# Kernel tuning notes

Measured on AMD Instinct MI355X. Metric: run time of the kernel, lower is better.

Reference implementation:

```python
import jax, jax.numpy as jnp
import numpy as np

INPUT_DIM = 1024
HIDDEN_DIM = 2048
LATENT_DIM = 256
NUM_EMBEDDINGS = 8192
COMMITMENT_COST = 0.25
BATCH = 16384


def setup_inputs() -> dict:
    key = jax.random.key(0)
    ks = jax.random.split(key, 10)
    def lin(k, fan_in, fan_out):
        # torch nn.Linear default init: U(-1/sqrt(fan_in), 1/sqrt(fan_in))
        bound = 1.0 / np.sqrt(fan_in)
        kw, kb = jax.random.split(k)
        W = jax.random.uniform(kw, (fan_in, fan_out), jnp.float32, -bound, bound)
        b = jax.random.uniform(kb, (fan_out,), jnp.float32, -bound, bound)
        return W, b
    enc_w1, enc_b1 = lin(ks[0], INPUT_DIM, HIDDEN_DIM)
    enc_w2, enc_b2 = lin(ks[1], HIDDEN_DIM, LATENT_DIM)
    dec_w1, dec_b1 = lin(ks[2], LATENT_DIM, HIDDEN_DIM)
    dec_w2, dec_b2 = lin(ks[3], HIDDEN_DIM, INPUT_DIM)
    # codebook init: U(-1/K, 1/K)
    codebook = jax.random.uniform(ks[4], (NUM_EMBEDDINGS, LATENT_DIM), jnp.float32,
                                  -1.0 / NUM_EMBEDDINGS, 1.0 / NUM_EMBEDDINGS)
    x = jax.random.uniform(ks[5], (BATCH, INPUT_DIM), jnp.float32)
    return {"x": x,
            "enc_w1": enc_w1, "enc_b1": enc_b1, "enc_w2": enc_w2, "enc_b2": enc_b2,
            "codebook": codebook,
            "dec_w1": dec_w1, "dec_b1": dec_b1, "dec_w2": dec_w2, "dec_b2": dec_b2}


def reference(x, enc_w1, enc_b1, enc_w2, enc_b2, codebook,
              dec_w1, dec_b1, dec_w2, dec_b2):
    # Encoder: relu(x W1 + b1) W2 + b2 -> z [N, latent]
    h = jax.nn.relu(x @ enc_w1 + enc_b1)
    z = h @ enc_w2 + enc_b2

    # Vector quantizer: squared-L2 distances to codebook [N, K]
    d = (jnp.sum(z * z, axis=1, keepdims=True)
         + jnp.sum(codebook * codebook, axis=1)
         - 2.0 * (z @ codebook.T))
    idx = jnp.argmin(d, axis=1)          # [N] int
    z_q = codebook[idx]                   # gather [N, latent]

    vq_loss = jnp.mean((jax.lax.stop_gradient(z_q) - z) ** 2)
    commit_loss = COMMITMENT_COST * jnp.mean((z_q - jax.lax.stop_gradient(z)) ** 2)
    loss = vq_loss + commit_loss

    # straight-through estimator
    z_q = z + jax.lax.stop_gradient(z_q - z)

    # Decoder: sigmoid(relu(z_q Wd1 + bd1) Wd2 + bd2)
    hd = jax.nn.relu(z_q @ dec_w1 + dec_b1)
    x_recon = jax.nn.sigmoid(hd @ dec_w2 + dec_b2)
    return (x_recon, loss)
```

## Files before the change

kernel.cpp:

```cpp
#include <hip/hip_runtime.h>
#include <math.h>

typedef unsigned short u16;
typedef __bf16 bf16x8 __attribute__((ext_vector_type(8)));
typedef float  f32x4  __attribute__((ext_vector_type(4)));

constexpr int B_  = 16384;
constexpr int DIN = 1024;
constexpr int DH  = 2048;
constexpr int DL  = 256;
constexpr int NE  = 8192;

__device__ __forceinline__ u16 f2bf(float f) {
    union { float f; unsigned u; } v; v.f = f;
    unsigned r = v.u + 0x7fffu + ((v.u >> 16) & 1u);
    return (u16)(r >> 16);
}
__device__ __forceinline__ float bf2f(u16 h) {
    union { unsigned u; float f; } v; v.u = ((unsigned)h) << 16;
    return v.f;
}

#define GLD16(gp, lp)                                                  \
    __builtin_amdgcn_global_load_lds(                                  \
        (__attribute__((address_space(1))) void*)(gp),                 \
        (__attribute__((address_space(3))) void*)(lp), 16, 0, 0)

#define SCHED0() __builtin_amdgcn_sched_barrier(0)
#define BARRIER() do { SCHED0(); __builtin_amdgcn_s_barrier(); SCHED0(); } while (0)
#define WAITV0() asm volatile("s_waitcnt vmcnt(0)" ::: "memory")
#define WAITV3() asm volatile("s_waitcnt vmcnt(3)" ::: "memory")
#define WAITV4() asm volatile("s_waitcnt vmcnt(4)" ::: "memory")

__global__ __launch_bounds__(256)
void cast_bf16(const float* __restrict__ in, u16* __restrict__ out)
{
    const size_t i = ((size_t)blockIdx.x * 256 + threadIdx.x) * 4;
    float4 v = *(const float4*)(in + i);
    ushort4 o;
    o.x = f2bf(v.x); o.y = f2bf(v.y); o.z = f2bf(v.z); o.w = f2bf(v.w);
    *(ushort4*)(out + i) = o;
}

__global__ __launch_bounds__(256)
void transpose_cast(const float* __restrict__ in, u16* __restrict__ out,
                    int R, int C)
{
    __shared__ float t[32][33];
    const int tx = threadIdx.x & 31, ty = threadIdx.x >> 5;
    const long bx = blockIdx.x;
    const long by = blockIdx.y;
#pragma unroll
    for (int p = 0; p < 4; ++p)
        t[ty + p * 8][tx] = in[(by * 32 + ty + p * 8) * (long)C + bx * 32 + tx];
    __syncthreads();
#pragma unroll
    for (int p = 0; p < 4; ++p)
        out[(bx * 32 + ty + p * 8) * (long)R + by * 32 + tx] = f2bf(t[tx][ty + p * 8]);
}

__global__ __launch_bounds__(256)
void cn2_kernel(const float* __restrict__ cb, float* __restrict__ cn2)
{
    const int code = (blockIdx.x * 256 + threadIdx.x) >> 6;
    const int lane = threadIdx.x & 63;
    float4 v = *(const float4*)(cb + (long)code * DL + lane * 4);
    float s = fmaf(v.x, v.x, fmaf(v.y, v.y, fmaf(v.z, v.z, v.w * v.w)));
#pragma unroll
    for (int off = 32; off; off >>= 1) s += __shfl_down(s, off);
    if (lane == 0) cn2[code] = 0.5f * s;
}

template <int EPI>
__global__ __launch_bounds__(512, 4)
void gemm_big_bf16(const u16* __restrict__ A, const u16* __restrict__ Bt,
                   const float* __restrict__ bias, void* __restrict__ Cout,
                   int M, int N, int K)
{
    __shared__ __align__(16) u16 As[3 * 8192];
    __shared__ __align__(16) u16 Bs[3 * 4096];

    const int tid = threadIdx.x;
    const int w = tid >> 6, l = tid & 63;
    const int wm = w >> 1, wn = w & 1;

    const int nbx   = N >> 7;
    const int nwg   = (M >> 8) * nbx;
    const int chunk = nwg >> 3;
    const int wg    = ((int)blockIdx.x & 7) * chunk + ((int)blockIdx.x >> 3);
    const long by   = wg / nbx;
    const long bx   = wg % nbx;

    const int lr  = l >> 2;
    const int lsw = (l & 3) ^ ((l >> 3) & 3);
    const int lg  = l >> 4, lm = l & 15;
    const int sx  = (lm >> 1) & 3;

    const u16* Abase = A  + (size_t)(by * 256) * K;
    const u16* Bbase = Bt + (size_t)(bx * 128) * K;

    f32x4 acc[4][4] = {};

    auto stage = [&](int k0, int b) {
        u16* dA = As + b * 8192;
        u16* dB = Bs + b * 4096;
#pragma unroll
        for (int i = 0; i < 2; ++i) {
            const int seg = w * 2 + i;
            GLD16(Abase + (size_t)(seg * 16 + lr) * K + k0 + lsw * 8,
                  dA + seg * 512);
        }
        GLD16(Bbase + (size_t)(w * 16 + lr) * K + k0 + lsw * 8,
              dB + w * 512);
    };

    const int NT = K >> 5;
    stage(0, 0);
    stage(32, 1);

    int cur = 0, pre = 2;
    for (int t = 0; t < NT; ++t) {
        if (t + 1 < NT) { WAITV3(); } else { WAITV0(); }
        BARRIER();
        if (t + 2 < NT) stage((t + 2) << 5, pre);

        const u16* as = As + cur * 8192;
        const u16* bs = Bs + cur * 4096;
        bf16x8 af[4], bfr[4];
#pragma unroll
        for (int m = 0; m < 4; ++m) {
            const int R = wm * 64 + m * 16 + lm;
            af[m] = *(const bf16x8*)&as[R * 32 + ((lg ^ sx) * 8)];
        }
#pragma unroll
        for (int n = 0; n < 4; ++n) {
            const int R = wn * 64 + n * 16 + lm;
            bfr[n] = *(const bf16x8*)&bs[R * 32 + ((lg ^ sx) * 8)];
        }
#pragma unroll
        for (int m = 0; m < 4; ++m)
#pragma unroll
            for (int n = 0; n < 4; ++n)
                acc[m][n] = __builtin_amdgcn_mfma_f32_16x16x32_bf16(
                    af[m], bfr[n], acc[m][n], 0, 0, 0);

        cur = (cur == 2) ? 0 : cur + 1;
        pre = (pre == 2) ? 0 : pre + 1;
    }

#pragma unroll
    for (int n = 0; n < 4; ++n) {
        const long col = bx * 128 + wn * 64 + n * 16 + lm;
        const float bb = bias[col];
#pragma unroll
        for (int m = 0; m < 4; ++m) {
#pragma unroll
            for (int j = 0; j < 4; ++j) {
                const long row = by * 256 + wm * 64 + m * 16 + lg * 4 + j;
                float e = acc[m][n][j] + bb;
                if (EPI == 1) e = fmaxf(e, 0.f);
                if (EPI == 2) {
                    e = 1.f / (1.f + expf(-e));
                    ((float*)Cout)[row * (long)N + col] = e;
                } else {
                    ((u16*)Cout)[row * (long)N + col] = f2bf(e);
                }
            }
        }
    }
}

template <int EPI>
__global__ __launch_bounds__(256)
void gemm_bt_bf16(const u16* __restrict__ A, const u16* __restrict__ Bt,
                  const float* __restrict__ bias, void* __restrict__ Cout,
                  int M, int N, int K)
{
    __shared__ __align__(16) u16 As[3 * 4096];
    __shared__ __align__(16) u16 Bs[3 * 4096];

    const int tid = threadIdx.x;
    const int w = tid >> 6, l = tid & 63;
    const int wr = w >> 1, wc = w & 1;

    const int nbx   = N >> 7;
    const int nwg   = (M >> 7) * nbx;
    const int chunk = nwg >> 3;
    const int wg    = ((int)blockIdx.x & 7) * chunk + ((int)blockIdx.x >> 3);
    const long by   = wg / nbx;
    const long bx   = wg % nbx;

    const int lr  = l >> 2;
    const int lsw = (l & 3) ^ ((l >> 3) & 3);
    const int lg  = l >> 4, lm = l & 15;
    const int sx  = (lm >> 1) & 3;

    const u16* Abase = A  + (size_t)(by * 128) * K;
    const u16* Bbase = Bt + (size_t)(bx * 128) * K;

    f32x4 acc[4][4] = {};

    auto stage = [&](int k0, int b) {
        u16* dA = As + b * 4096;
        u16* dB = Bs + b * 4096;
#pragma unroll
        for (int i = 0; i < 2; ++i) {
            const int seg = w * 2 + i;
            GLD16(Abase + (size_t)(seg * 16 + lr) * K + k0 + lsw * 8, dA + seg * 512);
            GLD16(Bbase + (size_t)(seg * 16 + lr) * K + k0 + lsw * 8, dB + seg * 512);
        }
    };

    const int NT = K >> 5;
    stage(0, 0);
    stage(32, 1);

    int cur = 0, pre = 2;
    for (int t = 0; t < NT; ++t) {
        if (t + 1 < NT) { WAITV4(); } else { WAITV0(); }
        BARRIER();
        if (t + 2 < NT) stage((t + 2) << 5, pre);

        const u16* as = As + cur * 4096;
        const u16* bs = Bs + cur * 4096;
        bf16x8 af[4], bfr[4];
#pragma unroll
        for (int m = 0; m < 4; ++m)
            af[m] = *(const bf16x8*)&as[(wr * 64 + m * 16 + lm) * 32 + ((lg ^ sx) * 8)];
#pragma unroll
        for (int n = 0; n < 4; ++n)
            bfr[n] = *(const bf16x8*)&bs[(wc * 64 + n * 16 + lm) * 32 + ((lg ^ sx) * 8)];
#pragma unroll
        for (int m = 0; m < 4; ++m)
#pragma unroll
            for (int n = 0; n < 4; ++n)
                acc[m][n] = __builtin_amdgcn_mfma_f32_16x16x32_bf16(
                    af[m], bfr[n], acc[m][n], 0, 0, 0);

        cur = (cur == 2) ? 0 : cur + 1;
        pre = (pre == 2) ? 0 : pre + 1;
    }

#pragma unroll
    for (int n = 0; n < 4; ++n) {
        const long col = bx * 128 + wc * 64 + n * 16 + lm;
        const float bb = bias[col];
#pragma unroll
        for (int m = 0; m < 4; ++m) {
#pragma unroll
            for (int j = 0; j < 4; ++j) {
                const long row = by * 128 + wr * 64 + m * 16 + lg * 4 + j;
                float e = acc[m][n][j] + bb;
                if (EPI == 1) e = fmaxf(e, 0.f);
                if (EPI == 2) {
                    e = 1.f / (1.f + expf(-e));
                    ((float*)Cout)[row * (long)N + col] = e;
                } else {
                    ((u16*)Cout)[row * (long)N + col] = f2bf(e);
                }
            }
        }
    }
}

__global__ __launch_bounds__(256, 2)
void vq_score2(const u16* __restrict__ z, const u16* __restrict__ cbt,
               const float* __restrict__ cn2,
               float* __restrict__ val8, int* __restrict__ idx8)
{
    __shared__ __align__(16) u16 lds[32768];

    const int tid = threadIdx.x;
    const int w = tid >> 6, l = tid & 63;
    const int rq = blockIdx.x >> 3;
    const int q  = blockIdx.x & 7;

    const int st_row8 = tid >> 5;
    const int st_s    = (tid & 31) ^ st_row8;
    const int lg = l >> 4, lm = l & 15;
    const int swz_x = l & 7;

    bf16x8 af[4][8];
    const long zbase_row = (long)rq * 256;
#pragma unroll
    for (int h = 0; h < 2; ++h) {
#pragma unroll
        for (int i = 0; i < 16; ++i) {
            const int row = i * 8 + st_row8;
            const u16* g = z + (zbase_row + h * 128 + row) * DL + st_s * 8;
            GLD16(g, lds + ((size_t)i * 256 + w * 64) * 8);
        }
        __syncthreads();
        if ((w >> 1) == h) {
            const int lrow0 = (w & 1) * 64;
#pragma unroll
            for (int m = 0; m < 4; ++m) {
                const int lrow = lrow0 + m * 16 + lm;
#pragma unroll
                for (int kg = 0; kg < 8; ++kg) {
                    const int s = (kg * 4 + lg) ^ swz_x;
                    af[m][kg] = *(const bf16x8*)&lds[lrow * 256 + s * 8];
                }
            }
        }
        __syncthreads();
    }

    const int code00 = q * (NE / 8);

    float bestv[16];
    int   besti[16];
#pragma unroll
    for (int k = 0; k < 16; ++k) { bestv[k] = 1e30f; besti[k] = 0; }

    auto stage_tile = [&](int t) {
        const int b = t & 1;
#pragma unroll
        for (int i = 0; i < 8; ++i) {
            const int c = i * 8 + st_row8;
            const u16* g = cbt + (size_t)(code00 + t * 64 + c) * DL + st_s * 8;
            GLD16(g, lds + ((size_t)b * 16384 + ((size_t)i * 256 + w * 64) * 8));
        }
    };

    stage_tile(0);
    __syncthreads();

    for (int t = 0; t < 16; ++t) {
        if (t < 15) stage_tile(t + 1);
        const u16* buf = lds + (size_t)(t & 1) * 16384;

#pragma unroll
        for (int n = 0; n < 4; ++n) {
            const int code_g = code00 + t * 64 + n * 16 + lm;
            const float cn2v = cn2[code_g];
            bf16x8 bfr[8];
#pragma unroll
            for (int kg = 0; kg < 8; ++kg) {
                const int lrow = n * 16 + lm;
                const int s = (kg * 4 + lg) ^ swz_x;
                bfr[kg] = *(const bf16x8*)&buf[lrow * 256 + s * 8];
            }
            f32x4 acc[4] = {};
#pragma unroll
            for (int kg = 0; kg < 8; ++kg)
#pragma unroll
                for (int m = 0; m < 4; ++m)
                    acc[m] = __builtin_amdgcn_mfma_f32_16x16x32_bf16(
                        af[m][kg], bfr[kg], acc[m], 0, 0, 0);
#pragma unroll
            for (int m = 0; m < 4; ++m)
#pragma unroll
                for (int j = 0; j < 4; ++j) {
                    const float s = cn2v - acc[m][j];
                    const int k16 = m * 4 + j;
                    if (s < bestv[k16]) { bestv[k16] = s; besti[k16] = code_g; }
                }
        }
        __syncthreads();
    }

#pragma unroll
    for (int off = 1; off < 16; off <<= 1) {
#pragma unroll
        for (int k = 0; k < 16; ++k) {
            const float ov = __shfl_xor(bestv[k], off);
            const int   oi = __shfl_xor(besti[k], off);
            if (ov < bestv[k] || (ov == bestv[k] && oi < besti[k])) {
                bestv[k] = ov; besti[k] = oi;
            }
        }
    }
    if (lm == 0) {
#pragma unroll
        for (int m = 0; m < 4; ++m)
#pragma unroll
            for (int j = 0; j < 4; ++j) {
                const long row = zbase_row + w * 64 + m * 16 + lg * 4 + j;
                val8[(size_t)q * B_ + row] = bestv[m * 4 + j];
                idx8[(size_t)q * B_ + row] = besti[m * 4 + j];
            }
    }
}

__global__ __launch_bounds__(256)
void vq_select2(const float* __restrict__ val8, const int* __restrict__ idx8,
                const u16* __restrict__ z, const float* __restrict__ cb,
                u16* __restrict__ zq, float* __restrict__ partial)
{
    __shared__ int   s_idx[256];
    __shared__ float s_red[4];
    const int tid = threadIdx.x;
    const long row = (long)blockIdx.x * 256 + tid;

    float bv = val8[row];
    int   bi = idx8[row];
#pragma unroll
    for (int qq = 1; qq < 8; ++qq) {
        const float v = val8[(size_t)qq * B_ + row];
        const int   i = idx8[(size_t)qq * B_ + row];
        if (v < bv || (v == bv && i < bi)) { bv = v; bi = i; }
    }
    s_idx[tid] = bi;
    __syncthreads();

    float ls = 0.f;
    const int sub = tid & 7;
#pragma unroll
    for (int pass = 0; pass < 8; ++pass) {
        const int rl = pass * 32 + (tid >> 3);
        const int gi = s_idx[rl];
        const long rg = (long)blockIdx.x * 256 + rl;
#pragma unroll
        for (int tt = 0; tt < 8; ++tt) {
            const int d = sub * 4 + tt * 32;
            float4 c4 = *(const float4*)(cb + (long)gi * DL + d);
            ushort4 zu = *(const ushort4*)(z + rg * DL + d);
            ushort4 qo;
            qo.x = f2bf(c4.x); qo.y = f2bf(c4.y);
            qo.z = f2bf(c4.z); qo.w = f2bf(c4.w);
            *(ushort4*)(zq + rg * DL + d) = qo;
            const float dx = c4.x - bf2f(zu.x), dy = c4.y - bf2f(zu.y);
            const float dz = c4.z - bf2f(zu.z), dw = c4.w - bf2f(zu.w);
            ls += dx * dx + dy * dy + dz * dz + dw * dw;
        }
    }
#pragma unroll
    for (int off = 32; off; off >>= 1) ls += __shfl_down(ls, off);
    if ((tid & 63) == 0) s_red[tid >> 6] = ls;
    __syncthreads();
    if (tid == 0)
        partial[blockIdx.x] = s_red[0] + s_red[1] + s_red[2] + s_red[3];
}

__global__ __launch_bounds__(256)
void loss_finalize(const float* __restrict__ partial, float* __restrict__ out)
{
    __shared__ float s_red[4];
    const int tid = threadIdx.x;
    float s = (tid < 64) ? partial[tid] : 0.f;
#pragma unroll
    for (int off = 32; off; off >>= 1) s += __shfl_down(s, off);
    if ((tid & 63) == 0) s_red[tid >> 6] = s;
    __syncthreads();
    if (tid == 0)
        out[0] = 1.25f * (s_red[0] + s_red[1] + s_red[2] + s_red[3])
                 / (float)((long)B_ * DL);
}

extern "C" void kernel_launch(void* const* d_in, const int* in_sizes, int n_in,
                              void* d_out, int out_size, void* d_ws, size_t ws_size,
                              hipStream_t stream)
{
    const float* x   = (const float*)d_in[0];
    const float* ew1 = (const float*)d_in[1];
    const float* eb1 = (const float*)d_in[2];
    const float* ew2 = (const float*)d_in[3];
    const float* eb2 = (const float*)d_in[4];
    const float* cbk = (const float*)d_in[5];
    const float* dw1 = (const float*)d_in[6];
    const float* db1 = (const float*)d_in[7];
    const float* dw2 = (const float*)d_in[8];
    const float* db2 = (const float*)d_in[9];
    float* out = (float*)d_out;

    char* p = (char*)d_ws;
    auto alloc = [&](size_t bytes) {
        char* r = p; p += (bytes + 255) & ~(size_t)255; return r;
    };
    u16*   x_bf  = (u16*)alloc((size_t)B_ * DIN * 2);
    u16*   h_bf  = (u16*)alloc((size_t)B_ * DH * 2);
    u16*   z_bf  = (u16*)alloc((size_t)B_ * DL * 2);
    u16*   zq_bf = (u16*)alloc((size_t)B_ * DL * 2);
    u16*   cb_bf = (u16*)alloc((size_t)NE * DL * 2);
    u16*   w1t   = (u16*)alloc((size_t)DH * DIN * 2);
    u16*   w2t   = (u16*)alloc((size_t)DL * DH * 2);
    u16*   wd1t  = (u16*)alloc((size_t)DH * DL * 2);
    u16*   wd2t  = (u16*)alloc((size_t)DIN * DH * 2);
    float* cn2   = (float*)alloc((size_t)NE * 4);
    float* val8  = (float*)alloc((size_t)8 * B_ * 4);
    int*   idx8  = (int*)alloc((size_t)8 * B_ * 4);
    float* part  = (float*)alloc(64 * 4);

    cast_bf16<<<(size_t)B_ * DIN / 1024, 256, 0, stream>>>(x, x_bf);
    cast_bf16<<<(size_t)NE * DL / 1024, 256, 0, stream>>>(cbk, cb_bf);
    transpose_cast<<<dim3(DH / 32, DIN / 32), 256, 0, stream>>>(ew1, w1t, DIN, DH);
    transpose_cast<<<dim3(DL / 32, DH / 32), 256, 0, stream>>>(ew2, w2t, DH, DL);
    transpose_cast<<<dim3(DH / 32, DL / 32), 256, 0, stream>>>(dw1, wd1t, DL, DH);
    transpose_cast<<<dim3(DIN / 32, DH / 32), 256, 0, stream>>>(dw2, wd2t, DH, DIN);
    cn2_kernel<<<NE / 4, 256, 0, stream>>>(cbk, cn2);

    gemm_big_bf16<1><<<(B_ / 256) * (DH / 128), 512, 0, stream>>>(
        x_bf, w1t, eb1, h_bf, B_, DH, DIN);
    gemm_bt_bf16<0><<<(B_ / 128) * (DL / 128), 256, 0, stream>>>(
        h_bf, w2t, eb2, z_bf, B_, DL, DH);

    vq_score2<<<512, 256, 0, stream>>>(z_bf, cb_bf, cn2, val8, idx8);
    vq_select2<<<B_ / 256, 256, 0, stream>>>(val8, idx8, z_bf, cbk, zq_bf, part);
    loss_finalize<<<1, 256, 0, stream>>>(part, out + (size_t)B_ * DIN);

    gemm_big_bf16<1><<<(B_ / 256) * (DH / 128), 512, 0, stream>>>(
        zq_bf, wd1t, db1, h_bf, B_, DH, DL);
    gemm_big_bf16<2><<<(B_ / 256) * (DIN / 128), 512, 0, stream>>>(
        h_bf, wd2t, db2, out, B_, DIN, DH);
}
```

Baseline: 337.2 us.

## Decode the codebook once and gather reconstructed rows by index

Because the decoder input is exactly a codebook row, the decoder MLP now runs on the 8192 codebook entries instead of the 16384 batch rows, and the final outputs are gathered per row using the argmin index. This halves the decoder GEMM work and removes the writing of the quantized latent. The cost is an extra fp32 table of decoded codebook rows and a gather pass over the full output. It is mathematically valid for any inputs, since batch rows mapping to the same code produce identical decoder outputs.

```diff
diff --git a/kernel.cpp b/kernel.cpp
--- a/kernel.cpp
+++ b/kernel.cpp
@@ -386,7 +386,7 @@
 __global__ __launch_bounds__(256)
 void vq_select2(const float* __restrict__ val8, const int* __restrict__ idx8,
                 const u16* __restrict__ z, const float* __restrict__ cb,
-                u16* __restrict__ zq, float* __restrict__ partial)
+                int* __restrict__ idxf, float* __restrict__ partial)
 {
     __shared__ int   s_idx[256];
     __shared__ float s_red[4];
@@ -402,6 +402,7 @@
         if (v < bv || (v == bv && i < bi)) { bv = v; bi = i; }
     }
     s_idx[tid] = bi;
+    idxf[row]  = bi;
     __syncthreads();
 
     float ls = 0.f;
@@ -416,10 +417,6 @@
             const int d = sub * 4 + tt * 32;
             float4 c4 = *(const float4*)(cb + (long)gi * DL + d);
             ushort4 zu = *(const ushort4*)(z + rg * DL + d);
-            ushort4 qo;
-            qo.x = f2bf(c4.x); qo.y = f2bf(c4.y);
-            qo.z = f2bf(c4.z); qo.w = f2bf(c4.w);
-            *(ushort4*)(zq + rg * DL + d) = qo;
             const float dx = c4.x - bf2f(zu.x), dy = c4.y - bf2f(zu.y);
             const float dz = c4.z - bf2f(zu.z), dw = c4.w - bf2f(zu.w);
             ls += dx * dx + dy * dy + dz * dz + dw * dw;
@@ -446,6 +443,23 @@
     if (tid == 0)
         out[0] = 1.25f * (s_red[0] + s_red[1] + s_red[2] + s_red[3])
                  / (float)((long)B_ * DL);
+}
+
+__global__ __launch_bounds__(256)
+void gather_rows(const float* __restrict__ Xcode, const int* __restrict__ idxf,
+                 float* __restrict__ out)
+{
+    const int tid  = threadIdx.x;
+    const int lane = tid & 63;
+    const long row = (long)blockIdx.x * 4 + (tid >> 6);
+    const long gi  = idxf[row];
+    const float* src = Xcode + gi * DIN;
+    float*       dst = out + row * DIN;
+#pragma unroll
+    for (int t = 0; t < 4; ++t) {
+        const int d = lane * 4 + t * 256;
+        *(float4*)(dst + d) = *(const float4*)(src + d);
+    }
 }
 
 extern "C" void kernel_launch(void* const* d_in, const int* in_sizes, int n_in,
@@ -471,15 +485,16 @@
     u16*   x_bf  = (u16*)alloc((size_t)B_ * DIN * 2);
     u16*   h_bf  = (u16*)alloc((size_t)B_ * DH * 2);
     u16*   z_bf  = (u16*)alloc((size_t)B_ * DL * 2);
-    u16*   zq_bf = (u16*)alloc((size_t)B_ * DL * 2);
     u16*   cb_bf = (u16*)alloc((size_t)NE * DL * 2);
     u16*   w1t   = (u16*)alloc((size_t)DH * DIN * 2);
     u16*   w2t   = (u16*)alloc((size_t)DL * DH * 2);
     u16*   wd1t  = (u16*)alloc((size_t)DH * DL * 2);
     u16*   wd2t  = (u16*)alloc((size_t)DIN * DH * 2);
+    float* Xcode = (float*)alloc((size_t)NE * DIN * 4);
     float* cn2   = (float*)alloc((size_t)NE * 4);
     float* val8  = (float*)alloc((size_t)8 * B_ * 4);
     int*   idx8  = (int*)alloc((size_t)8 * B_ * 4);
+    int*   idxf  = (int*)alloc((size_t)B_ * 4);
     float* part  = (float*)alloc(64 * 4);
 
     cast_bf16<<<(size_t)B_ * DIN / 1024, 256, 0, stream>>>(x, x_bf);
@@ -496,11 +511,12 @@
         h_bf, w2t, eb2, z_bf, B_, DL, DH);
 
     vq_score2<<<512, 256, 0, stream>>>(z_bf, cb_bf, cn2, val8, idx8);
-    vq_select2<<<B_ / 256, 256, 0, stream>>>(val8, idx8, z_bf, cbk, zq_bf, part);
+    vq_select2<<<B_ / 256, 256, 0, stream>>>(val8, idx8, z_bf, cbk, idxf, part);
     loss_finalize<<<1, 256, 0, stream>>>(part, out + (size_t)B_ * DIN);
 
-    gemm_big_bf16<1><<<(B_ / 256) * (DH / 128), 512, 0, stream>>>(
-        zq_bf, wd1t, db1, h_bf, B_, DH, DL);
-    gemm_big_bf16<2><<<(B_ / 256) * (DIN / 128), 512, 0, stream>>>(
-        h_bf, wd2t, db2, out, B_, DIN, DH);
-}
+    gemm_big_bf16<1><<<(NE / 256) * (DH / 128), 512, 0, stream>>>(
+        cb_bf, wd1t, db1, h_bf, NE, DH, DL);
+    gemm_big_bf16<2><<<(NE / 256) * (DIN / 128), 512, 0, stream>>>(
+        h_bf, wd2t, db2, Xcode, NE, DIN, DH);
+    gather_rows<<<B_ / 4, 256, 0, stream>>>(Xcode, idxf, out);
+}
```

Result: faster. 324.7 us (-3.7%).
